# Performance work log

Measured on AMD Instinct MI355X. Metric: run time of the kernel, lower is better.

## Reference

```python
import jax, jax.numpy as jnp
import numpy as np

_FRAC_BITS = 8  # assumed fixed-point fractional bits for bits_quant
_SCALE = float(2 ** _FRAC_BITS)

def bits_quant(x):
    # Simulated fixed-point quantization: round to nearest multiple of 2^-8.
    return jnp.round(x * _SCALE) / _SCALE


def setup_inputs() -> dict:
    key = jax.random.key(0)
    k1, k2, k3 = jax.random.split(key, 3)
    B, D_in, D_out = 4096, 4096, 4096
    inputs = jax.random.normal(k1, (B, D_in), dtype=jnp.float32)
    w = jax.random.normal(k2, (D_in, D_out), dtype=jnp.float32) * 0.02
    b = jax.random.normal(k3, (D_out,), dtype=jnp.float32) * 0.02
    return {"inputs": inputs, "w": w, "b": b}


def reference(inputs, w, b):
    # y = bits_quant(inputs @ w) + bits_quant(b); out = bits_quant(y)
    y = bits_quant(jnp.matmul(inputs, w)) + bits_quant(b)
    return bits_quant(y)
```

## Files before the change

kernel.cpp:

```cpp
#include <hip/hip_runtime.h>
#include <math.h>

typedef __attribute__((ext_vector_type(8)))  short  short8;
typedef __attribute__((ext_vector_type(16))) float  f32x16;
typedef __attribute__((ext_vector_type(4)))  float  float4v;
typedef __attribute__((ext_vector_type(8)))  unsigned short ushort8;
typedef __attribute__((ext_vector_type(4)))  unsigned short ushort4v;

#define NDIM 4096
#define BM 256
#define BN 256
#define BK 64
#define T_TILES (NDIM / BK)
#define IMG_USH 8192

__device__ __forceinline__ unsigned short f2bf(float f) {
  unsigned u = __builtin_bit_cast(unsigned, f);
  u += 0x7fffu + ((u >> 16) & 1u);
  return (unsigned short)(u >> 16);
}

__device__ __forceinline__ void gload_lds16(const unsigned short* g, unsigned short* l) {
  __builtin_amdgcn_global_load_lds(
      (const __attribute__((address_space(1))) void*)g,
      (__attribute__((address_space(3))) void*)l, 16, 0, 0);
}

__global__ __launch_bounds__(256)
void prep(const float* __restrict__ A, unsigned short* __restrict__ Abf,
          const float* __restrict__ W, unsigned short* __restrict__ Wt) {
  const int t = threadIdx.x;
  if (blockIdx.x < 2048) {
    const int b  = blockIdx.x;
    const int mb = b >> 6, kt = b & 63;
    const int h  = (t >> 6) & 3, fh = (t >> 5) & 1, fr = t & 31;
    const float* src0 = A + (size_t)(mb * 128 + fr) * NDIM + kt * 64 + h * 16 + fh * 8;
    unsigned short* dst = Abf + ((size_t)(mb * 64 + kt) * 1024 + t) * 8;
#pragma unroll
    for (int p = 0; p < 4; ++p) {
      const float* s = src0 + (size_t)(p * 32) * NDIM;
      float4v a = *(const float4v*)s;
      float4v c = *(const float4v*)(s + 4);
      ushort8 o;
      o[0] = f2bf(a[0]); o[1] = f2bf(a[1]); o[2] = f2bf(a[2]); o[3] = f2bf(a[3]);
      o[4] = f2bf(c[0]); o[5] = f2bf(c[1]); o[6] = f2bf(c[2]); o[7] = f2bf(c[3]);
      *(ushort8*)(dst + (size_t)p * 2048) = o;
    }
  } else {
    const int b  = blockIdx.x - 2048;
    const int nb = b >> 6, kt = b & 63;
    const int n0 = (t & 31) * 4;
    const int kq = t >> 5;
    float4v v[8];
#pragma unroll
    for (int r = 0; r < 8; ++r)
      v[r] = *(const float4v*)&W[(size_t)(kt * 64 + kq * 8 + r) * NDIM + nb * 128 + n0];
    const int q  = (t & 31) >> 3;
    const int h  = kq >> 1, fh = kq & 1;
    unsigned short* img = Wt + (size_t)(nb * 64 + kt) * IMG_USH;
#pragma unroll
    for (int c = 0; c < 4; ++c) {
      const int fr = (n0 + c) & 31;
      ushort8 o;
#pragma unroll
      for (int r = 0; r < 8; ++r) o[r] = f2bf(v[r][c]);
      *(ushort8*)(img + ((size_t)((q * 4 + h) * 64 + fh * 32 + fr)) * 8) = o;
    }
  }
}

__global__ __launch_bounds__(512, 1)
void gemm_bt_quant(const unsigned short* __restrict__ Abf,
                   const unsigned short* __restrict__ Wt,
                   const float* __restrict__ bias,
                   float* __restrict__ C) {
  __shared__ unsigned short lds[8 * IMG_USH];

  const int tid  = threadIdx.x;
  const int lane = tid & 63;
  const int wid  = tid >> 6;
  const int wr   = wid >> 2;
  const int wc   = wid & 3;
  const int hb   = wc >> 1;

  const int bid  = blockIdx.y * 16 + blockIdx.x;
  const int swz  = (bid & 7) * 32 + (bid >> 3);
  const int m0   = (swz >> 4) * BM;
  const int n0   = (swz & 15) * BN;
  const int mb0  = (swz >> 4) * 2;
  const int nb0  = (swz & 15) * 2;

  const unsigned short* Aimg = Abf + (size_t)mb0 * 64 * IMG_USH;
  const unsigned short* Bimg = Wt  + (size_t)nb0 * 64 * IMG_USH;

  auto stageA = [&](int u, int ha) {
    unsigned short* dst = &lds[(ha * 2 + (u & 1)) * IMG_USH];
    const unsigned short* src = Aimg + ((size_t)(ha * 64 + u)) * IMG_USH + tid * 8;
    gload_lds16(src,        dst + tid * 8);
    gload_lds16(src + 4096, dst + 4096 + tid * 8);
  };
  auto stageB = [&](int u, int h2) {
    unsigned short* dst = &lds[(4 + h2 * 2 + (u & 1)) * IMG_USH];
    const unsigned short* src = Bimg + ((size_t)(h2 * 64 + u)) * IMG_USH + tid * 8;
    gload_lds16(src,        dst + tid * 8);
    gload_lds16(src + 4096, dst + 4096 + tid * 8);
  };

  f32x16 acc[4][2] = {};

  stageB(0, 0); stageB(0, 1);
  stageA(0, 0); stageA(0, 1);
  stageB(1, 0); stageB(1, 1);
  asm volatile("s_waitcnt vmcnt(4)" ::: "memory");
  __builtin_amdgcn_s_barrier();

  const int lofs = lane * 8;

  for (int u = 0; u < T_TILES; ++u) {
    const unsigned short* Ah = &lds[(wr * 2 + (u & 1)) * IMG_USH];
    const unsigned short* Bh = &lds[(4 + hb * 2 + (u & 1)) * IMG_USH + (wc & 1) * 4096];
    short8 bk[2][4];
#pragma unroll
    for (int p = 0; p < 4; ++p) {
      if (p == 0) {
#pragma unroll
        for (int j = 0; j < 2; ++j)
#pragma unroll
          for (int h = 0; h < 4; ++h)
            bk[j][h] = *(const short8*)&Bh[j * 2048 + h * 512 + lofs];
      }
      short8 af[4];
#pragma unroll
      for (int h = 0; h < 4; ++h)
        af[h] = *(const short8*)&Ah[p * 2048 + h * 512 + lofs];

      if (p == 0 && u + 1 < T_TILES) stageA(u + 1, 0);
      if (p == 1 && u + 1 < T_TILES) stageA(u + 1, 1);
      if (p == 2 && u + 2 < T_TILES) stageB(u + 2, 0);
      if (p == 3 && u + 2 < T_TILES) stageB(u + 2, 1);

      __builtin_amdgcn_sched_barrier(0);
      if (p == 3) {
        if (u < T_TILES - 2) asm volatile("s_waitcnt vmcnt(4)" ::: "memory");
        else                 asm volatile("s_waitcnt vmcnt(0)" ::: "memory");
      }
      __builtin_amdgcn_s_barrier();
      asm volatile("s_waitcnt lgkmcnt(0)" ::: "memory");
      __builtin_amdgcn_sched_barrier(0);
      __builtin_amdgcn_s_setprio(1);
#pragma unroll
      for (int h = 0; h < 4; ++h)
#pragma unroll
        for (int j = 0; j < 2; ++j)
          acc[p][j] = __builtin_amdgcn_mfma_f32_32x32x16_bf16(af[h], bk[j][h], acc[p][j], 0, 0, 0);
      __builtin_amdgcn_s_setprio(0);
      __builtin_amdgcn_s_barrier();
      __builtin_amdgcn_sched_barrier(0);
    }
  }

  const int fr = lane & 31;
  const int fh = lane >> 5;
  const float inv = 1.0f / 256.0f;
#pragma unroll
  for (int j = 0; j < 2; ++j) {
    const int col = n0 + wc * 64 + j * 32 + fr;
    const float qb = rintf(bias[col] * 256.0f) * inv;
#pragma unroll
    for (int p = 0; p < 4; ++p) {
      const int rb = m0 + wr * 128 + p * 32 + 4 * fh;
#pragma unroll
      for (int r = 0; r < 16; ++r) {
        const int row = rb + (r & 3) + 8 * (r >> 2);
        C[(size_t)row * NDIM + col] = rintf(acc[p][j][r] * 256.0f) * inv + qb;
      }
    }
  }
}

__global__ void gemm_fb(const float* __restrict__ A, const float* __restrict__ W,
                        const float* __restrict__ bias, float* __restrict__ C) {
  __shared__ float As[32][33], Ws[32][33];
  int tx = threadIdx.x, ty = threadIdx.y;
  int m0 = blockIdx.y * 32, n0 = blockIdx.x * 32;
  float acc[4] = {0.f, 0.f, 0.f, 0.f};
  for (int k0 = 0; k0 < NDIM; k0 += 32) {
#pragma unroll
    for (int i = 0; i < 4; ++i) {
      int r = ty + i * 8;
      As[r][tx] = A[(size_t)(m0 + r) * NDIM + k0 + tx];
      Ws[r][tx] = W[(size_t)(k0 + r) * NDIM + n0 + tx];
    }
    __syncthreads();
#pragma unroll
    for (int k = 0; k < 32; ++k) {
      float wv = Ws[k][tx];
#pragma unroll
      for (int i = 0; i < 4; ++i) acc[i] += As[ty + i * 8][k] * wv;
    }
    __syncthreads();
  }
  float qb = rintf(bias[n0 + tx] * 256.0f) * (1.0f / 256.0f);
#pragma unroll
  for (int i = 0; i < 4; ++i)
    C[(size_t)(m0 + ty + i * 8) * NDIM + n0 + tx] =
        rintf(acc[i] * 256.0f) * (1.0f / 256.0f) + qb;
}

extern "C" void kernel_launch(void* const* d_in, const int* in_sizes, int n_in,
                              void* d_out, int out_size, void* d_ws, size_t ws_size,
                              hipStream_t stream) {
  const float* A    = (const float*)d_in[0];
  const float* W    = (const float*)d_in[1];
  const float* bias = (const float*)d_in[2];
  float* C = (float*)d_out;
  const size_t nElem = (size_t)NDIM * NDIM;

  if (ws_size >= nElem * 4) {
    unsigned short* Abf = (unsigned short*)d_ws;
    unsigned short* Wt  = Abf + nElem;
    prep<<<4096, 256, 0, stream>>>(A, Abf, W, Wt);
    gemm_bt_quant<<<dim3(16, 16), 512, 0, stream>>>(Abf, Wt, bias, C);
  } else {
    gemm_fb<<<dim3(128, 128), dim3(32, 8), 0, stream>>>(A, W, bias, C);
  }
}
```

Measured before the change: 295.9 us.

## Software-pipeline LDS fragment loads and cut per-tile barriers in GEMM main loop

```diff
diff --git a/kernel.cpp b/kernel.cpp
--- a/kernel.cpp
+++ b/kernel.cpp
@@ -69,7 +69,7 @@
   }
 }
 
-__global__ __launch_bounds__(512, 1)
+__global__ __launch_bounds__(512, 2)
 void gemm_bt_quant(const unsigned short* __restrict__ Abf,
                    const unsigned short* __restrict__ Wt,
                    const float* __restrict__ bias,
@@ -93,15 +93,15 @@
   const unsigned short* Aimg = Abf + (size_t)mb0 * 64 * IMG_USH;
   const unsigned short* Bimg = Wt  + (size_t)nb0 * 64 * IMG_USH;
 
-  auto stageA = [&](int u, int ha) {
-    unsigned short* dst = &lds[(ha * 2 + (u & 1)) * IMG_USH];
-    const unsigned short* src = Aimg + ((size_t)(ha * 64 + u)) * IMG_USH + tid * 8;
+  auto stageA = [&](int t2, int ha) {
+    unsigned short* dst = &lds[((t2 & 1) * 2 + ha) * IMG_USH];
+    const unsigned short* src = Aimg + ((size_t)(ha * 64 + t2)) * IMG_USH + tid * 8;
     gload_lds16(src,        dst + tid * 8);
     gload_lds16(src + 4096, dst + 4096 + tid * 8);
   };
-  auto stageB = [&](int u, int h2) {
-    unsigned short* dst = &lds[(4 + h2 * 2 + (u & 1)) * IMG_USH];
-    const unsigned short* src = Bimg + ((size_t)(h2 * 64 + u)) * IMG_USH + tid * 8;
+  auto stageB = [&](int t2, int h2) {
+    unsigned short* dst = &lds[(4 + (t2 & 1) * 2 + h2) * IMG_USH];
+    const unsigned short* src = Bimg + ((size_t)(h2 * 64 + t2)) * IMG_USH + tid * 8;
     gload_lds16(src,        dst + tid * 8);
     gload_lds16(src + 4096, dst + 4096 + tid * 8);
   };
@@ -113,47 +113,77 @@
   stageB(1, 0); stageB(1, 1);
   asm volatile("s_waitcnt vmcnt(4)" ::: "memory");
   __builtin_amdgcn_s_barrier();
+  __builtin_amdgcn_sched_barrier(0);
 
   const int lofs = lane * 8;
 
   for (int u = 0; u < T_TILES; ++u) {
-    const unsigned short* Ah = &lds[(wr * 2 + (u & 1)) * IMG_USH];
-    const unsigned short* Bh = &lds[(4 + hb * 2 + (u & 1)) * IMG_USH + (wc & 1) * 4096];
-    short8 bk[2][4];
-#pragma unroll
-    for (int p = 0; p < 4; ++p) {
-      if (p == 0) {
-#pragma unroll
-        for (int j = 0; j < 2; ++j)
-#pragma unroll
-          for (int h = 0; h < 4; ++h)
-            bk[j][h] = *(const short8*)&Bh[j * 2048 + h * 512 + lofs];
-      }
-      short8 af[4];
+    const unsigned short* Ah = &lds[((u & 1) * 2 + wr) * IMG_USH];
+    const unsigned short* Bh = &lds[(4 + (u & 1) * 2 + hb) * IMG_USH + (wc & 1) * 4096];
+    short8 bk[2][4], af0[4], af1[4], af2[4], af3[4];
+
+#pragma unroll
+    for (int j = 0; j < 2; ++j)
 #pragma unroll
       for (int h = 0; h < 4; ++h)
-        af[h] = *(const short8*)&Ah[p * 2048 + h * 512 + lofs];
-
-      if (p == 0 && u + 1 < T_TILES) stageA(u + 1, 0);
-      if (p == 1 && u + 1 < T_TILES) stageA(u + 1, 1);
-      if (p == 2 && u + 2 < T_TILES) stageB(u + 2, 0);
-      if (p == 3 && u + 2 < T_TILES) stageB(u + 2, 1);
-
-      __builtin_amdgcn_sched_barrier(0);
-      if (p == 3) {
-        if (u < T_TILES - 2) asm volatile("s_waitcnt vmcnt(4)" ::: "memory");
-        else                 asm volatile("s_waitcnt vmcnt(0)" ::: "memory");
-      }
-      __builtin_amdgcn_s_barrier();
-      asm volatile("s_waitcnt lgkmcnt(0)" ::: "memory");
-      __builtin_amdgcn_sched_barrier(0);
-      __builtin_amdgcn_s_setprio(1);
-#pragma unroll
-      for (int h = 0; h < 4; ++h)
-#pragma unroll
-        for (int j = 0; j < 2; ++j)
-          acc[p][j] = __builtin_amdgcn_mfma_f32_32x32x16_bf16(af[h], bk[j][h], acc[p][j], 0, 0, 0);
-      __builtin_amdgcn_s_setprio(0);
+        bk[j][h] = *(const short8*)&Bh[j * 2048 + h * 512 + lofs];
+#pragma unroll
+    for (int h = 0; h < 4; ++h)
+      af0[h] = *(const short8*)&Ah[0 * 2048 + h * 512 + lofs];
+    if (u + 1 < T_TILES) stageA(u + 1, 0);
+#pragma unroll
+    for (int h = 0; h < 4; ++h)
+      af1[h] = *(const short8*)&Ah[1 * 2048 + h * 512 + lofs];
+    __builtin_amdgcn_s_setprio(1);
+#pragma unroll
+    for (int h = 0; h < 4; ++h)
+#pragma unroll
+      for (int j = 0; j < 2; ++j)
+        acc[0][j] = __builtin_amdgcn_mfma_f32_32x32x16_bf16(af0[h], bk[j][h], acc[0][j], 0, 0, 0);
+    __builtin_amdgcn_s_setprio(0);
+    __builtin_amdgcn_sched_barrier(0);
+
+    if (u + 1 < T_TILES) stageA(u + 1, 1);
+#pragma unroll
+    for (int h = 0; h < 4; ++h)
+      af2[h] = *(const short8*)&Ah[2 * 2048 + h * 512 + lofs];
+    __builtin_amdgcn_s_setprio(1);
+#pragma unroll
+    for (int h = 0; h < 4; ++h)
+#pragma unroll
+      for (int j = 0; j < 2; ++j)
+        acc[1][j] = __builtin_amdgcn_mfma_f32_32x32x16_bf16(af1[h], bk[j][h], acc[1][j], 0, 0, 0);
+    __builtin_amdgcn_s_setprio(0);
+    __builtin_amdgcn_sched_barrier(0);
+
+    __builtin_amdgcn_s_barrier();
+    __builtin_amdgcn_sched_barrier(0);
+
+    if (u + 2 < T_TILES) stageB(u + 2, 0);
+#pragma unroll
+    for (int h = 0; h < 4; ++h)
+      af3[h] = *(const short8*)&Ah[3 * 2048 + h * 512 + lofs];
+    __builtin_amdgcn_s_setprio(1);
+#pragma unroll
+    for (int h = 0; h < 4; ++h)
+#pragma unroll
+      for (int j = 0; j < 2; ++j)
+        acc[2][j] = __builtin_amdgcn_mfma_f32_32x32x16_bf16(af2[h], bk[j][h], acc[2][j], 0, 0, 0);
+    __builtin_amdgcn_s_setprio(0);
+    __builtin_amdgcn_sched_barrier(0);
+
+    if (u + 2 < T_TILES) stageB(u + 2, 1);
+    __builtin_amdgcn_s_setprio(1);
+#pragma unroll
+    for (int h = 0; h < 4; ++h)
+#pragma unroll
+      for (int j = 0; j < 2; ++j)
+        acc[3][j] = __builtin_amdgcn_mfma_f32_32x32x16_bf16(af3[h], bk[j][h], acc[3][j], 0, 0, 0);
+    __builtin_amdgcn_s_setprio(0);
+
+    if (u < T_TILES - 1) {
+      if (u < T_TILES - 2) asm volatile("s_waitcnt vmcnt(4)" ::: "memory");
+      else                 asm volatile("s_waitcnt vmcnt(0)" ::: "memory");
       __builtin_amdgcn_s_barrier();
       __builtin_amdgcn_sched_barrier(0);
     }
```

Result: no change. 298.0 us (+0.7%).
